# Kernel optimization log

Hardware: AMD Instinct MI355X
Metric: run time of the kernel (lower is better)

## Reference

```python
import jax, jax.numpy as jnp
import numpy as np

NUM_USERS, NUM_ITEMS, NUM_BRANDS = 100000, 50000, 1000
N = NUM_USERS + NUM_ITEMS + NUM_BRANDS  # 151000 total graph nodes
E = 4_800_000                           # nnz of normalized adjacency
D, D_CONTENT = 64, 384
N_LAYERS = 3


def setup_inputs() -> dict:
    key = jax.random.key(0)
    ks = jax.random.split(key, 9)
    return {
        "edge_row": jax.random.randint(ks[0], (E,), 0, N, dtype=jnp.int32),
        "edge_col": jax.random.randint(ks[1], (E,), 0, N, dtype=jnp.int32),
        "edge_val": jax.random.uniform(ks[2], (E,), dtype=jnp.float32),
        "user_emb": jax.random.normal(ks[3], (NUM_USERS, D), dtype=jnp.float32) * 0.1,
        "item_id_emb": jax.random.normal(ks[4], (NUM_ITEMS, D), dtype=jnp.float32) * 0.1,
        "brand_emb": jax.random.normal(ks[5], (NUM_BRANDS, D), dtype=jnp.float32) * 0.1,
        "item_content_emb": jax.random.normal(ks[6], (NUM_ITEMS, D_CONTENT), dtype=jnp.float32),
        "fusion_W": jax.random.normal(ks[7], (D, D + D_CONTENT), dtype=jnp.float32) * 0.05,
        "fusion_b": jnp.zeros((D,), dtype=jnp.float32),
    }


def _spmm(edge_row, edge_col, edge_val, x):
    # out[i] = sum_{e: row[e]==i} val[e] * x[col[e]]  -- COO SpMM via segment_sum
    msgs = edge_val[:, None] * x[edge_col]  # [E, D]
    return jax.ops.segment_sum(msgs, edge_row, num_segments=N)


def reference(edge_row, edge_col, edge_val, user_emb, item_id_emb, brand_emb,
              item_content_emb, fusion_W, fusion_b):
    # Fuse item-id embedding with frozen content embedding, then LeakyReLU
    combined = jnp.concatenate([item_id_emb, item_content_emb], axis=1)  # [I, D+Dc]
    fused_item = jax.nn.leaky_relu(combined @ fusion_W.T + fusion_b, negative_slope=0.01)

    ego = jnp.concatenate([user_emb, fused_item, brand_emb], axis=0)  # [N, D]
    acc = ego
    for _ in range(N_LAYERS):
        ego = _spmm(edge_row, edge_col, edge_val, ego)
        acc = acc + ego
    final = acc / jnp.asarray(N_LAYERS + 1, dtype=acc.dtype)  # layer-mean pooling

    final_user = final[:NUM_USERS]
    final_item = final[NUM_USERS:NUM_USERS + NUM_ITEMS]
    final_brand = final[NUM_USERS + NUM_ITEMS:]
    return final_user, final_item, final_brand, user_emb, item_id_emb
```

## Files before the change

### kernel.cpp

```cpp
#include <hip/hip_runtime.h>
#include <hip/hip_fp16.h>

#define NU 100000
#define NI 50000
#define NB 1000
#define NN 151000
#define NE 4800000
#define KDIM 448

#define BROW_BITS 9
#define BROWS 512
#define NBK ((NN + BROWS - 1) / BROWS)

typedef float v2f __attribute__((ext_vector_type(2)));

__device__ __forceinline__ unsigned int pk_fp8x4(float a, float b, float c, float d) {
  int r = 0;
  r = __builtin_amdgcn_cvt_pk_fp8_f32(a, b, r, false);
  r = __builtin_amdgcn_cvt_pk_fp8_f32(c, d, r, true);
  return (unsigned int)r;
}

#define HIST_EPT 16
__global__ __launch_bounds__(256) void bucket_hist(const int* __restrict__ erow,
                                                   int* __restrict__ bcnt) {
  __shared__ int lh[NBK];
  for (int i = threadIdx.x; i < NBK; i += 256) lh[i] = 0;
  __syncthreads();
  int base = blockIdx.x * (256 * HIST_EPT) + threadIdx.x;
#pragma unroll
  for (int j = 0; j < HIST_EPT; ++j) {
    int e = base + j * 256;
    if (e < NE) atomicAdd(&lh[erow[e] >> BROW_BITS], 1);
  }
  __syncthreads();
  for (int i = threadIdx.x; i < NBK; i += 256) {
    int c = lh[i];
    if (c) atomicAdd(&bcnt[i], c);
  }
}

__global__ __launch_bounds__(256) void bucket_scan(const int* __restrict__ bcnt,
                                                   int* __restrict__ bstart,
                                                   int* __restrict__ rp) {
  __shared__ int sh[256];
  int tid = threadIdx.x;
  int v[2];
  int s = 0;
#pragma unroll
  for (int j = 0; j < 2; ++j) {
    int i = tid * 2 + j;
    v[j] = (i < NBK) ? bcnt[i] : 0;
    s += v[j];
  }
  sh[tid] = s;
  __syncthreads();
  for (int off = 1; off < 256; off <<= 1) {
    int t = (tid >= off) ? sh[tid - off] : 0;
    __syncthreads();
    sh[tid] += t;
    __syncthreads();
  }
  int run = sh[tid] - s;
#pragma unroll
  for (int j = 0; j < 2; ++j) {
    int i = tid * 2 + j;
    if (i < NBK) bstart[i] = run;
    run += v[j];
  }
  if (tid == 255) {
    bstart[NBK] = NE;
    rp[NN] = NE;
  }
}

#define SC_EPT 32
__global__ __launch_bounds__(256) void bucket_scatter(
    const int* __restrict__ erow, const int* __restrict__ ecol,
    const float* __restrict__ eval, const int* __restrict__ bstart,
    int* __restrict__ gfill, int2* __restrict__ cvtmp) {
  __shared__ int lcnt[NBK];
  __shared__ int lbase[NBK];
  __shared__ unsigned short lrank[256 * SC_EPT];
  for (int i = threadIdx.x; i < NBK; i += 256) lcnt[i] = 0;
  __syncthreads();
  int base = blockIdx.x * (256 * SC_EPT) + threadIdx.x;
  int rv[SC_EPT];
#pragma unroll
  for (int j = 0; j < SC_EPT; ++j) {
    int e = base + j * 256;
    if (e < NE) {
      int r = erow[e];
      rv[j] = r;
      lrank[j * 256 + threadIdx.x] = (unsigned short)atomicAdd(&lcnt[r >> BROW_BITS], 1);
    } else {
      rv[j] = -1;
    }
  }
  __syncthreads();
  for (int i = threadIdx.x; i < NBK; i += 256) {
    int c = lcnt[i];
    lbase[i] = c ? atomicAdd(&gfill[i], c) : 0;
  }
  __syncthreads();
#pragma unroll
  for (int j = 0; j < SC_EPT; ++j) {
    int e = base + j * 256;
    if (e < NE) {
      int r = rv[j];
      int c = ecol[e];
      float v = eval[e];
      int bk = r >> BROW_BITS;
      int key = ((r & (BROWS - 1)) << 18) | c;
      int p = bstart[bk] + lbase[bk] + lrank[j * 256 + threadIdx.x];
      cvtmp[p] = make_int2(key, __float_as_int(v));
    }
  }
}

__global__ __launch_bounds__(256) void csr_finalize(
    const int* __restrict__ bstart, const int2* __restrict__ cvtmp,
    int* __restrict__ rp, int2* __restrict__ cv) {
  __shared__ int rcnt[BROWS];
  __shared__ int rex[BROWS];
  __shared__ int ssh[256];
  int b = blockIdx.x;
  int s0 = bstart[b], s1 = bstart[b + 1];
  int tid = threadIdx.x;
  rcnt[tid] = 0;
  rcnt[tid + 256] = 0;
  __syncthreads();
  for (int j = s0 + tid; j < s1; j += 256) atomicAdd(&rcnt[cvtmp[j].x >> 18], 1);
  __syncthreads();
  int v0 = rcnt[2 * tid], v1 = rcnt[2 * tid + 1];
  int tsum = v0 + v1;
  ssh[tid] = tsum;
  __syncthreads();
  for (int off = 1; off < 256; off <<= 1) {
    int t = (tid >= off) ? ssh[tid - off] : 0;
    __syncthreads();
    ssh[tid] += t;
    __syncthreads();
  }
  int excl = ssh[tid] - tsum;
  rex[2 * tid] = excl;
  rex[2 * tid + 1] = excl + v0;
  int row = b * BROWS + 2 * tid;
  if (row < NN) rp[row] = s0 + excl;
  if (row + 1 < NN) rp[row + 1] = s0 + excl + v0;
  rcnt[2 * tid] = 0;
  rcnt[2 * tid + 1] = 0;
  __syncthreads();
  for (int j = s0 + tid; j < s1; j += 256) {
    int2 kv = cvtmp[j];
    int r = kv.x >> 18;
    int c = kv.x & 0x3FFFF;
    int rk = atomicAdd(&rcnt[r], 1);
    cv[s0 + rex[r] + rk] = make_int2(c, kv.y);
  }
}

__global__ __launch_bounds__(256) void fusion_kernel(
    const float* __restrict__ id_emb, const float* __restrict__ content,
    const float* __restrict__ W, const float* __restrict__ bias,
    unsigned char* __restrict__ x8, float* __restrict__ out) {
  __shared__ float As[16][68];
  __shared__ float Ws[16][68];
  int tid = threadIdx.x;
  int tx = tid & 15;
  int ty = tid >> 4;
  int itemBase = blockIdx.x * 64;
  float acc[4][4] = {};

  int it = tid >> 2;
  int kq = (tid & 3) * 4;

  for (int kb = 0; kb < KDIM; kb += 16) {
    int k = kb + kq;
    int item = itemBase + it;
    int itemc = item < NI ? item : NI - 1;
    float4 a;
    if (k < 64)
      a = *(const float4*)&id_emb[(size_t)itemc * 64 + k];
    else
      a = *(const float4*)&content[(size_t)itemc * 384 + (k - 64)];
    As[kq + 0][it] = a.x; As[kq + 1][it] = a.y; As[kq + 2][it] = a.z; As[kq + 3][it] = a.w;
    float4 w = *(const float4*)&W[(size_t)it * KDIM + k];
    Ws[kq + 0][it] = w.x; Ws[kq + 1][it] = w.y; Ws[kq + 2][it] = w.z; Ws[kq + 3][it] = w.w;
    __syncthreads();
#pragma unroll
    for (int kk = 0; kk < 16; ++kk) {
      float4 af = *(float4*)&As[kk][ty * 4];
      float4 wf = *(float4*)&Ws[kk][tx * 4];
      float av[4] = {af.x, af.y, af.z, af.w};
      float wv[4] = {wf.x, wf.y, wf.z, wf.w};
#pragma unroll
      for (int m = 0; m < 4; ++m)
#pragma unroll
        for (int n = 0; n < 4; ++n) acc[m][n] += av[m] * wv[n];
    }
    __syncthreads();
  }

  int d0 = tx * 4;
  float4 bb = *(const float4*)&bias[d0];
#pragma unroll
  for (int m = 0; m < 4; ++m) {
    int item = itemBase + ty * 4 + m;
    if (item >= NI) continue;
    float4 o;
    float t;
    t = acc[m][0] + bb.x; o.x = t >= 0.f ? t : 0.01f * t;
    t = acc[m][1] + bb.y; o.y = t >= 0.f ? t : 0.01f * t;
    t = acc[m][2] + bb.z; o.z = t >= 0.f ? t : 0.01f * t;
    t = acc[m][3] + bb.w; o.w = t >= 0.f ? t : 0.01f * t;
    size_t ofs = (size_t)(NU + item) * 64 + d0;
    *(float4*)&out[ofs] = o;
    *(unsigned int*)&x8[ofs] = pk_fp8x4(o.x, o.y, o.z, o.w);
  }
}

#define UN (NU * 64)
#define BN (NB * 64)
#define IEL (NI * 64)
__global__ __launch_bounds__(256) void seed_kernel(
    const float* __restrict__ user_emb, const float* __restrict__ brand,
    const float* __restrict__ item_id, unsigned char* __restrict__ x8,
    float* __restrict__ out) {
  int idx = (blockIdx.x * 256 + threadIdx.x) * 4;
  if (idx < UN) {
    float4 f = *(const float4*)&user_emb[idx];
    *(float4*)&out[idx] = f;
    *(float4*)&out[(size_t)NN * 64 + idx] = f;
    *(unsigned int*)&x8[idx] = pk_fp8x4(f.x, f.y, f.z, f.w);
  } else if (idx < UN + BN) {
    int k = idx - UN;
    float4 f = *(const float4*)&brand[k];
    int o = (NU + NI) * 64 + k;
    *(float4*)&out[o] = f;
    *(unsigned int*)&x8[o] = pk_fp8x4(f.x, f.y, f.z, f.w);
  } else if (idx < UN + BN + IEL) {
    int k = idx - (UN + BN);
    float4 f = *(const float4*)&item_id[k];
    *(float4*)&out[(size_t)(NN + NU) * 64 + k] = f;
  }
}

template <bool FINAL>
__global__ __launch_bounds__(256) void spmm_kernel(
    const int* __restrict__ rp, const int2* __restrict__ cv,
    const unsigned char* __restrict__ x, unsigned char* __restrict__ y,
    float* __restrict__ acc) {
  int wid = blockIdx.x * 4 + (threadIdx.x >> 6);
  if (wid >= NN) return;
  int lane = threadIdx.x & 63;
  int grp = lane >> 4;
  int d0 = (lane & 15) << 2;
  const unsigned char* __restrict__ xb = x + d0;
  int beg = rp[wid], end = rp[wid + 1];
  float a0 = 0.f, a1 = 0.f, a2 = 0.f, a3 = 0.f;
  float b0 = 0.f, b1 = 0.f, b2 = 0.f, b3 = 0.f;
  int j = beg + grp;
  for (; j + 12 < end; j += 16) {
    int2 p0 = cv[j];
    int2 p1 = cv[j + 4];
    int2 p2 = cv[j + 8];
    int2 p3 = cv[j + 12];
    unsigned int h0 = *(const unsigned int*)(xb + ((size_t)p0.x << 6));
    unsigned int h1 = *(const unsigned int*)(xb + ((size_t)p1.x << 6));
    unsigned int h2 = *(const unsigned int*)(xb + ((size_t)p2.x << 6));
    unsigned int h3 = *(const unsigned int*)(xb + ((size_t)p3.x << 6));
    float v0 = __int_as_float(p0.y);
    float v1 = __int_as_float(p1.y);
    float v2 = __int_as_float(p2.y);
    float v3 = __int_as_float(p3.y);
    v2f f;
    f = __builtin_amdgcn_cvt_pk_f32_fp8(h0, false); a0 += v0 * f.x; a1 += v0 * f.y;
    f = __builtin_amdgcn_cvt_pk_f32_fp8(h0, true);  a2 += v0 * f.x; a3 += v0 * f.y;
    f = __builtin_amdgcn_cvt_pk_f32_fp8(h1, false); b0 += v1 * f.x; b1 += v1 * f.y;
    f = __builtin_amdgcn_cvt_pk_f32_fp8(h1, true);  b2 += v1 * f.x; b3 += v1 * f.y;
    f = __builtin_amdgcn_cvt_pk_f32_fp8(h2, false); a0 += v2 * f.x; a1 += v2 * f.y;
    f = __builtin_amdgcn_cvt_pk_f32_fp8(h2, true);  a2 += v2 * f.x; a3 += v2 * f.y;
    f = __builtin_amdgcn_cvt_pk_f32_fp8(h3, false); b0 += v3 * f.x; b1 += v3 * f.y;
    f = __builtin_amdgcn_cvt_pk_f32_fp8(h3, true);  b2 += v3 * f.x; b3 += v3 * f.y;
  }
  for (; j < end; j += 4) {
    int2 p = cv[j];
    unsigned int h = *(const unsigned int*)(xb + ((size_t)p.x << 6));
    float v = __int_as_float(p.y);
    v2f f;
    f = __builtin_amdgcn_cvt_pk_f32_fp8(h, false); a0 += v * f.x; a1 += v * f.y;
    f = __builtin_amdgcn_cvt_pk_f32_fp8(h, true);  a2 += v * f.x; a3 += v * f.y;
  }
  a0 += b0; a1 += b1; a2 += b2; a3 += b3;
  a0 += __shfl_xor(a0, 16); a1 += __shfl_xor(a1, 16);
  a2 += __shfl_xor(a2, 16); a3 += __shfl_xor(a3, 16);
  a0 += __shfl_xor(a0, 32); a1 += __shfl_xor(a1, 32);
  a2 += __shfl_xor(a2, 32); a3 += __shfl_xor(a3, 32);
  if (lane < 16) {
    int o = (wid << 6) | d0;
    if (FINAL) {
      float4 t = *(const float4*)&acc[o];
      t.x = (t.x + a0) * 0.25f;
      t.y = (t.y + a1) * 0.25f;
      t.z = (t.z + a2) * 0.25f;
      t.w = (t.w + a3) * 0.25f;
      *(float4*)&acc[o] = t;
    } else {
      *(unsigned int*)&y[o] = pk_fp8x4(a0, a1, a2, a3);
      float4 t = *(const float4*)&acc[o];
      t.x += a0; t.y += a1; t.z += a2; t.w += a3;
      *(float4*)&acc[o] = t;
    }
  }
}

extern "C" void kernel_launch(void* const* d_in, const int* in_sizes, int n_in,
                              void* d_out, int out_size, void* d_ws, size_t ws_size,
                              hipStream_t stream) {
  const int*   edge_row = (const int*)d_in[0];
  const int*   edge_col = (const int*)d_in[1];
  const float* edge_val = (const float*)d_in[2];
  const float* user_emb = (const float*)d_in[3];
  const float* item_id  = (const float*)d_in[4];
  const float* brand    = (const float*)d_in[5];
  const float* content  = (const float*)d_in[6];
  const float* W        = (const float*)d_in[7];
  const float* bias     = (const float*)d_in[8];
  float* out = (float*)d_out;

  char* ws = (char*)d_ws;
  size_t off = 0;
  auto alloc = [&](size_t bytes) -> void* {
    void* p = ws + off;
    off += (bytes + 255) & ~(size_t)255;
    return p;
  };
  unsigned char* x8_0 = (unsigned char*)alloc((size_t)NN * 64);
  unsigned char* x8_1 = (unsigned char*)alloc((size_t)NN * 64);
  int2*   cvtmp = (int2*)alloc((size_t)NE * 8);
  int2*   cv    = (int2*)alloc((size_t)NE * 8);
  int*    rp    = (int*)alloc((size_t)(NN + 1) * 4);
  int*    bcnt  = (int*)alloc((NBK + 1) * 4);
  int*    bstart= (int*)alloc((NBK + 1) * 4);
  int*    gfill = (int*)alloc((NBK + 1) * 4);
  if (off > ws_size) return;

  hipMemsetAsync(bcnt, 0, (size_t)((char*)gfill - (char*)bcnt) + (NBK + 1) * 4,
                 stream);
  const int histBlocks = (NE + 256 * HIST_EPT - 1) / (256 * HIST_EPT);
  bucket_hist<<<histBlocks, 256, 0, stream>>>(edge_row, bcnt);
  bucket_scan<<<1, 256, 0, stream>>>(bcnt, bstart, rp);
  const int scBlocks = (NE + 256 * SC_EPT - 1) / (256 * SC_EPT);
  bucket_scatter<<<scBlocks, 256, 0, stream>>>(edge_row, edge_col, edge_val,
                                               bstart, gfill, cvtmp);
  csr_finalize<<<NBK, 256, 0, stream>>>(bstart, cvtmp, rp, cv);

  fusion_kernel<<<(NI + 63) / 64, 256, 0, stream>>>(item_id, content, W, bias,
                                                    x8_0, out);
  const int seedTot = UN + BN + IEL;
  seed_kernel<<<(seedTot / 4 + 255) / 256, 256, 0, stream>>>(user_emb, brand,
                                                             item_id, x8_0, out);

  const int spmmGrid = (NN + 3) / 4;
  spmm_kernel<false><<<spmmGrid, 256, 0, stream>>>(rp, cv, x8_0, x8_1, out);
  spmm_kernel<false><<<spmmGrid, 256, 0, stream>>>(rp, cv, x8_1, x8_0, out);
  spmm_kernel<true><<<spmmGrid, 256, 0, stream>>>(rp, cv, x8_0, x8_1, out);
}
```

Baseline: 722.3 us.

## Build CSR with per-row global atomics instead of two-pass bucket sort

Replaces the bucketed two-pass COO-to-CSR build (block-local bucket histogram, scatter into a temp buffer, per-bucket finalize) with a direct per-row histogram using global atomics, a hierarchical scan, and a single scatter that places each edge at its final position via a per-row atomic fill counter. This removes the intermediate 38MB temp buffer and one full read/write pass over the edges. In exchange it issues millions of global atomics on random rows and produces a nondeterministic within-row edge order, which can change floating-point summation order.

```diff
diff --git a/kernel.cpp b/kernel.cpp
--- a/kernel.cpp
+++ b/kernel.cpp
@@ -8,7 +8,6 @@
 #define NE 4800000
 #define KDIM 448
 
-#define BROW_BITS 9
 #define BROWS 512
 #define NBK ((NN + BROWS - 1) / BROWS)
 
@@ -21,23 +20,33 @@
   return (unsigned int)r;
 }
 
-#define HIST_EPT 16
-__global__ __launch_bounds__(256) void bucket_hist(const int* __restrict__ erow,
-                                                   int* __restrict__ bcnt) {
-  __shared__ int lh[NBK];
-  for (int i = threadIdx.x; i < NBK; i += 256) lh[i] = 0;
+#define RH_EPT 8
+__global__ __launch_bounds__(256) void row_hist(const int* __restrict__ erow,
+                                                int* __restrict__ rcnt) {
+  int base = blockIdx.x * (256 * RH_EPT) + threadIdx.x;
+#pragma unroll
+  for (int j = 0; j < RH_EPT; ++j) {
+    int e = base + j * 256;
+    if (e < NE) atomicAdd(&rcnt[erow[e]], 1);
+  }
+}
+
+__global__ __launch_bounds__(256) void bucket_sum(const int* __restrict__ rcnt,
+                                                  int* __restrict__ bcnt) {
+  __shared__ int sh[256];
+  int b = blockIdx.x;
+  int tid = threadIdx.x;
+  int i = b * BROWS + 2 * tid;
+  int s = 0;
+  if (i < NN) s += rcnt[i];
+  if (i + 1 < NN) s += rcnt[i + 1];
+  sh[tid] = s;
   __syncthreads();
-  int base = blockIdx.x * (256 * HIST_EPT) + threadIdx.x;
-#pragma unroll
-  for (int j = 0; j < HIST_EPT; ++j) {
-    int e = base + j * 256;
-    if (e < NE) atomicAdd(&lh[erow[e] >> BROW_BITS], 1);
-  }
-  __syncthreads();
-  for (int i = threadIdx.x; i < NBK; i += 256) {
-    int c = lh[i];
-    if (c) atomicAdd(&bcnt[i], c);
-  }
+  for (int off = 128; off > 0; off >>= 1) {
+    if (tid < off) sh[tid] += sh[tid + off];
+    __syncthreads();
+  }
+  if (tid == 0) bcnt[b] = sh[0];
 }
 
 __global__ __launch_bounds__(256) void bucket_scan(const int* __restrict__ bcnt,
@@ -74,89 +83,43 @@
   }
 }
 
-#define SC_EPT 32
-__global__ __launch_bounds__(256) void bucket_scatter(
+__global__ __launch_bounds__(256) void row_scan(const int* __restrict__ rcnt,
+                                                const int* __restrict__ bstart,
+                                                int* __restrict__ rp) {
+  __shared__ int sh[256];
+  int b = blockIdx.x;
+  int tid = threadIdx.x;
+  int i0 = b * BROWS + 2 * tid;
+  int v0 = (i0 < NN) ? rcnt[i0] : 0;
+  int v1 = (i0 + 1 < NN) ? rcnt[i0 + 1] : 0;
+  int s = v0 + v1;
+  sh[tid] = s;
+  __syncthreads();
+  for (int off = 1; off < 256; off <<= 1) {
+    int t = (tid >= off) ? sh[tid - off] : 0;
+    __syncthreads();
+    sh[tid] += t;
+    __syncthreads();
+  }
+  int excl = sh[tid] - s + bstart[b];
+  if (i0 < NN) rp[i0] = excl;
+  if (i0 + 1 < NN) rp[i0 + 1] = excl + v0;
+}
+
+#define RS_EPT 8
+__global__ __launch_bounds__(256) void row_scatter(
     const int* __restrict__ erow, const int* __restrict__ ecol,
-    const float* __restrict__ eval, const int* __restrict__ bstart,
-    int* __restrict__ gfill, int2* __restrict__ cvtmp) {
-  __shared__ int lcnt[NBK];
-  __shared__ int lbase[NBK];
-  __shared__ unsigned short lrank[256 * SC_EPT];
-  for (int i = threadIdx.x; i < NBK; i += 256) lcnt[i] = 0;
-  __syncthreads();
-  int base = blockIdx.x * (256 * SC_EPT) + threadIdx.x;
-  int rv[SC_EPT];
-#pragma unroll
-  for (int j = 0; j < SC_EPT; ++j) {
+    const float* __restrict__ eval, const int* __restrict__ rp,
+    int* __restrict__ gfill, int2* __restrict__ cv) {
+  int base = blockIdx.x * (256 * RS_EPT) + threadIdx.x;
+#pragma unroll
+  for (int j = 0; j < RS_EPT; ++j) {
     int e = base + j * 256;
     if (e < NE) {
       int r = erow[e];
-      rv[j] = r;
-      lrank[j * 256 + threadIdx.x] = (unsigned short)atomicAdd(&lcnt[r >> BROW_BITS], 1);
-    } else {
-      rv[j] = -1;
+      int p = rp[r] + atomicAdd(&gfill[r], 1);
+      cv[p] = make_int2(ecol[e], __float_as_int(eval[e]));
     }
-  }
-  __syncthreads();
-  for (int i = threadIdx.x; i < NBK; i += 256) {
-    int c = lcnt[i];
-    lbase[i] = c ? atomicAdd(&gfill[i], c) : 0;
-  }
-  __syncthreads();
-#pragma unroll
-  for (int j = 0; j < SC_EPT; ++j) {
-    int e = base + j * 256;
-    if (e < NE) {
-      int r = rv[j];
-      int c = ecol[e];
-      float v = eval[e];
-      int bk = r >> BROW_BITS;
-      int key = ((r & (BROWS - 1)) << 18) | c;
-      int p = bstart[bk] + lbase[bk] + lrank[j * 256 + threadIdx.x];
-      cvtmp[p] = make_int2(key, __float_as_int(v));
-    }
-  }
-}
-
-__global__ __launch_bounds__(256) void csr_finalize(
-    const int* __restrict__ bstart, const int2* __restrict__ cvtmp,
-    int* __restrict__ rp, int2* __restrict__ cv) {
-  __shared__ int rcnt[BROWS];
-  __shared__ int rex[BROWS];
-  __shared__ int ssh[256];
-  int b = blockIdx.x;
-  int s0 = bstart[b], s1 = bstart[b + 1];
-  int tid = threadIdx.x;
-  rcnt[tid] = 0;
-  rcnt[tid + 256] = 0;
-  __syncthreads();
-  for (int j = s0 + tid; j < s1; j += 256) atomicAdd(&rcnt[cvtmp[j].x >> 18], 1);
-  __syncthreads();
-  int v0 = rcnt[2 * tid], v1 = rcnt[2 * tid + 1];
-  int tsum = v0 + v1;
-  ssh[tid] = tsum;
-  __syncthreads();
-  for (int off = 1; off < 256; off <<= 1) {
-    int t = (tid >= off) ? ssh[tid - off] : 0;
-    __syncthreads();
-    ssh[tid] += t;
-    __syncthreads();
-  }
-  int excl = ssh[tid] - tsum;
-  rex[2 * tid] = excl;
-  rex[2 * tid + 1] = excl + v0;
-  int row = b * BROWS + 2 * tid;
-  if (row < NN) rp[row] = s0 + excl;
-  if (row + 1 < NN) rp[row + 1] = s0 + excl + v0;
-  rcnt[2 * tid] = 0;
-  rcnt[2 * tid + 1] = 0;
-  __syncthreads();
-  for (int j = s0 + tid; j < s1; j += 256) {
-    int2 kv = cvtmp[j];
-    int r = kv.x >> 18;
-    int c = kv.x & 0x3FFFF;
-    int rk = atomicAdd(&rcnt[r], 1);
-    cv[s0 + rex[r] + rk] = make_int2(c, kv.y);
   }
 }
 
@@ -338,23 +301,24 @@
   };
   unsigned char* x8_0 = (unsigned char*)alloc((size_t)NN * 64);
   unsigned char* x8_1 = (unsigned char*)alloc((size_t)NN * 64);
-  int2*   cvtmp = (int2*)alloc((size_t)NE * 8);
   int2*   cv    = (int2*)alloc((size_t)NE * 8);
   int*    rp    = (int*)alloc((size_t)(NN + 1) * 4);
+  int*    rcnt  = (int*)alloc((size_t)NN * 4);
+  int*    gfill = (int*)alloc((size_t)NN * 4);
   int*    bcnt  = (int*)alloc((NBK + 1) * 4);
   int*    bstart= (int*)alloc((NBK + 1) * 4);
-  int*    gfill = (int*)alloc((NBK + 1) * 4);
   if (off > ws_size) return;
 
-  hipMemsetAsync(bcnt, 0, (size_t)((char*)gfill - (char*)bcnt) + (NBK + 1) * 4,
+  hipMemsetAsync(rcnt, 0, (size_t)((char*)gfill - (char*)rcnt) + (size_t)NN * 4,
                  stream);
-  const int histBlocks = (NE + 256 * HIST_EPT - 1) / (256 * HIST_EPT);
-  bucket_hist<<<histBlocks, 256, 0, stream>>>(edge_row, bcnt);
+  const int rhBlocks = (NE + 256 * RH_EPT - 1) / (256 * RH_EPT);
+  row_hist<<<rhBlocks, 256, 0, stream>>>(edge_row, rcnt);
+  bucket_sum<<<NBK, 256, 0, stream>>>(rcnt, bcnt);
   bucket_scan<<<1, 256, 0, stream>>>(bcnt, bstart, rp);
-  const int scBlocks = (NE + 256 * SC_EPT - 1) / (256 * SC_EPT);
-  bucket_scatter<<<scBlocks, 256, 0, stream>>>(edge_row, edge_col, edge_val,
-                                               bstart, gfill, cvtmp);
-  csr_finalize<<<NBK, 256, 0, stream>>>(bstart, cvtmp, rp, cv);
+  row_scan<<<NBK, 256, 0, stream>>>(rcnt, bstart, rp);
+  const int rsBlocks = (NE + 256 * RS_EPT - 1) / (256 * RS_EPT);
+  row_scatter<<<rsBlocks, 256, 0, stream>>>(edge_row, edge_col, edge_val, rp,
+                                            gfill, cv);
 
   fusion_kernel<<<(NI + 63) / 64, 256, 0, stream>>>(item_id, content, W, bias,
                                                     x8_0, out);
```

Result: slower. 960.4 us (+33.0%).

## Stage bucket scatter in LDS so global writes are bucket-contiguous

Applied to the files above, without the earlier changes.

The bucket scatter kernel now sorts each block's edges by bucket in shared memory, using a local prefix scan over bucket counts, before writing them out. Consecutive threads then write consecutive slots within each bucket's global range, which coalesces the scattered int2 stores to cvtmp. Edges per thread drop from 32 to 8, so each block handles fewer edges and there are more blocks, more gfill atomics and a per-block scan over roughly 295 buckets. With only about 2048 edges spread across that many buckets per block, runs per bucket are short and the coalescing gain may be limited.

```diff
diff --git a/kernel.cpp b/kernel.cpp
--- a/kernel.cpp
+++ b/kernel.cpp
@@ -74,46 +74,76 @@
   }
 }
 
-#define SC_EPT 32
+#define SC_EPT 8
 __global__ __launch_bounds__(256) void bucket_scatter(
     const int* __restrict__ erow, const int* __restrict__ ecol,
     const float* __restrict__ eval, const int* __restrict__ bstart,
     int* __restrict__ gfill, int2* __restrict__ cvtmp) {
   __shared__ int lcnt[NBK];
+  __shared__ int lofs[NBK];
   __shared__ int lbase[NBK];
-  __shared__ unsigned short lrank[256 * SC_EPT];
-  for (int i = threadIdx.x; i < NBK; i += 256) lcnt[i] = 0;
-  __syncthreads();
-  int base = blockIdx.x * (256 * SC_EPT) + threadIdx.x;
-  int rv[SC_EPT];
+  __shared__ int ssh[256];
+  __shared__ int2 ekv[256 * SC_EPT];
+  __shared__ unsigned short bkid[256 * SC_EPT];
+  int tid = threadIdx.x;
+  for (int i = tid; i < NBK; i += 256) lcnt[i] = 0;
+  __syncthreads();
+  int base = blockIdx.x * (256 * SC_EPT) + tid;
+  int r_[SC_EPT], c_[SC_EPT], rk_[SC_EPT];
+  float v_[SC_EPT];
 #pragma unroll
   for (int j = 0; j < SC_EPT; ++j) {
     int e = base + j * 256;
     if (e < NE) {
       int r = erow[e];
-      rv[j] = r;
-      lrank[j * 256 + threadIdx.x] = (unsigned short)atomicAdd(&lcnt[r >> BROW_BITS], 1);
+      r_[j] = r;
+      c_[j] = ecol[e];
+      v_[j] = eval[e];
+      rk_[j] = atomicAdd(&lcnt[r >> BROW_BITS], 1);
     } else {
-      rv[j] = -1;
-    }
-  }
-  __syncthreads();
-  for (int i = threadIdx.x; i < NBK; i += 256) {
+      r_[j] = -1; c_[j] = 0; v_[j] = 0.f; rk_[j] = 0;
+    }
+  }
+  __syncthreads();
+  int a0 = (tid * 2 < NBK) ? lcnt[tid * 2] : 0;
+  int a1 = (tid * 2 + 1 < NBK) ? lcnt[tid * 2 + 1] : 0;
+  int s = a0 + a1;
+  ssh[tid] = s;
+  __syncthreads();
+  for (int off = 1; off < 256; off <<= 1) {
+    int t = (tid >= off) ? ssh[tid - off] : 0;
+    __syncthreads();
+    ssh[tid] += t;
+    __syncthreads();
+  }
+  int excl = ssh[tid] - s;
+  if (tid * 2 < NBK) lofs[tid * 2] = excl;
+  if (tid * 2 + 1 < NBK) lofs[tid * 2 + 1] = excl + a0;
+  for (int i = tid; i < NBK; i += 256) {
     int c = lcnt[i];
     lbase[i] = c ? atomicAdd(&gfill[i], c) : 0;
   }
   __syncthreads();
 #pragma unroll
   for (int j = 0; j < SC_EPT; ++j) {
-    int e = base + j * 256;
-    if (e < NE) {
-      int r = rv[j];
-      int c = ecol[e];
-      float v = eval[e];
+    int r = r_[j];
+    if (r >= 0) {
       int bk = r >> BROW_BITS;
-      int key = ((r & (BROWS - 1)) << 18) | c;
-      int p = bstart[bk] + lbase[bk] + lrank[j * 256 + threadIdx.x];
-      cvtmp[p] = make_int2(key, __float_as_int(v));
+      int slot = lofs[bk] + rk_[j];
+      ekv[slot] = make_int2(((r & (BROWS - 1)) << 18) | c_[j],
+                            __float_as_int(v_[j]));
+      bkid[slot] = (unsigned short)bk;
+    }
+  }
+  __syncthreads();
+  int total = ssh[255];
+#pragma unroll
+  for (int j = 0; j < SC_EPT; ++j) {
+    int slot = tid + j * 256;
+    if (slot < total) {
+      int bk = bkid[slot];
+      int p = bstart[bk] + lbase[bk] + (slot - lofs[bk]);
+      cvtmp[p] = ekv[slot];
     }
   }
 }
```

Result: faster. 694.4 us (-3.9%).
